# Kernel optimization log

Hardware: AMD Instinct MI355X
Metric: run time of the kernel (lower is better)

## Reference

```python
import jax, jax.numpy as jnp
import numpy as np

N = 50000      # nodes
E = 1600000    # edges (avg degree 32)
C_IN = 128
C_H = 128
C_OUT = 10
G = 512        # number of graphs in the batch


def setup_inputs() -> dict:
    key = jax.random.key(0)
    ks = jax.random.split(key, 16)
    x = jax.random.normal(ks[0], (N, C_IN), dtype=jnp.float32)
    edge_index = jax.random.randint(ks[1], (2, E), 0, N, dtype=jnp.int64)
    batch = jnp.sort(jax.random.randint(ks[2], (N,), 0, G, dtype=jnp.int64))

    def lin(k, fan_in, fan_out):
        lim = 1.0 / np.sqrt(fan_in)
        return jax.random.uniform(k, (fan_in, fan_out), jnp.float32, -lim, lim)

    return {
        "x": x, "edge_index": edge_index, "batch": batch,
        # conv1: c_in -> c_hidden
        "Wr1": lin(ks[3], C_IN, C_H), "br1": jnp.zeros((C_H,), jnp.float32),
        "Wo1": lin(ks[4], C_IN, C_H),
        # conv2: c_hidden -> 2*c_hidden
        "Wr2": lin(ks[5], C_H, 2 * C_H), "br2": jnp.zeros((2 * C_H,), jnp.float32),
        "Wo2": lin(ks[6], C_H, 2 * C_H),
        # conv3: 2*c_hidden -> c_hidden
        "Wr3": lin(ks[7], 2 * C_H, C_H), "br3": jnp.zeros((C_H,), jnp.float32),
        "Wo3": lin(ks[8], 2 * C_H, C_H),
        # head
        "W1": lin(ks[9], C_H, 4 * C_OUT), "b1": jnp.zeros((4 * C_OUT,), jnp.float32),
        "W2": lin(ks[10], 4 * C_OUT, C_OUT), "b2": jnp.zeros((C_OUT,), jnp.float32),
    }


def _graph_conv(x, src, dst, Wr, br, Wo):
    # PyG GraphConv: lin_rel(sum_{j in N(i)} x_j) + lin_root(x_i)
    agg = jax.ops.segment_sum(x[src], dst, num_segments=N)  # [N, F_in]
    return agg @ Wr + br + x @ Wo


def reference(x, edge_index, batch, Wr1, br1, Wo1, Wr2, br2, Wo2,
              Wr3, br3, Wo3, W1, b1, W2, b2):
    src, dst = edge_index[0], edge_index[1]
    h = jax.nn.relu(_graph_conv(x, src, dst, Wr1, br1, Wo1))
    h = jax.nn.relu(_graph_conv(h, src, dst, Wr2, br2, Wo2))
    h = _graph_conv(h, src, dst, Wr3, br3, Wo3)
    # global mean pool over graphs
    sums = jax.ops.segment_sum(h, batch, num_segments=G)            # [G, C_H]
    cnts = jax.ops.segment_sum(jnp.ones((N,), h.dtype), batch, num_segments=G)
    pooled = sums / jnp.maximum(cnts, 1.0)[:, None]
    # dropout is identity in eval mode
    out = pooled @ W1 + b1
    out = out @ W2 + b2
    return out
```

## Files before the change

### kernel.cpp

```cpp
#include <hip/hip_runtime.h>
#include <hip/hip_bf16.h>
#include <cstddef>

#define NN 50000
#define EE 1600000
#define GG 512
#define NB 196
#define BSTRIDE 16384
#define BCAP 10240
#define XBLKS 6250
#define SCBLKS 782
#define PSEG 8

typedef unsigned int u32;
typedef unsigned short u16;
typedef __attribute__((ext_vector_type(8))) short frag_ab;
typedef __attribute__((ext_vector_type(4))) float frag_cd;

__device__ __forceinline__ void gl_lds16(const void* g, void* l) {
    __builtin_amdgcn_global_load_lds(
        (const __attribute__((address_space(1))) u32*)g,
        (__attribute__((address_space(3))) u32*)l, 16, 0, 0);
}
__device__ __forceinline__ float b2f_lo(u32 v) { return __uint_as_float(v << 16); }
__device__ __forceinline__ float b2f_hi(u32 v) { return __uint_as_float(v & 0xffff0000u); }
__device__ __forceinline__ float b2f(u32 v, int odd) { return odd ? b2f_hi(v) : b2f_lo(v); }
__device__ __forceinline__ u16 f2b(float x) {
    __hip_bfloat16 h = __float2bfloat16(x);
    return *(u16*)&h;
}
__device__ __forceinline__ u32 pack2(float lo, float hi) {
    return ((u32)f2b(hi) << 16) | f2b(lo);
}
__device__ __forceinline__ void acc2(float2& a, u32 v) {
    a.x += b2f_lo(v);
    a.y += b2f_hi(v);
}

__device__ inline int lower_bound_i(const int* a, int n, int v) {
    int lo = 0, hi = n;
    while (lo < hi) {
        int m = (lo + hi) >> 1;
        if (a[m] < v) lo = m + 1; else hi = m;
    }
    return lo;
}



__global__ __launch_bounds__(256) void bscatter_prep_kernel(
    const int* __restrict__ ei, int* __restrict__ bcnt, u32* __restrict__ pairs,
    const float* __restrict__ x, u16* __restrict__ ax,
    const float* __restrict__ Wr1, const float* __restrict__ Wo1,
    const float* __restrict__ Wr2, const float* __restrict__ Wo2,
    const float* __restrict__ Wr3, const float* __restrict__ Wo3,
    const float* __restrict__ br3,
    u16* __restrict__ BT1, u16* __restrict__ BT2, u16* __restrict__ BT3,
    float* __restrict__ bias3, const int* __restrict__ batch,
    int* __restrict__ gn) {
    __shared__ int lcnt[NB];
    __shared__ int lbase[NB];
    __shared__ unsigned short lpos[2048];
    int bid = blockIdx.x, t = threadIdx.x;
    if (bid < SCBLKS) {
        int e0 = bid * 2048;
        u32 pk[8];
        int bk[8];
        for (int i = t; i < NB; i += 256) lcnt[i] = 0;
        __syncthreads();
#pragma unroll
        for (int i = 0; i < 8; ++i) {
            int e = e0 + i * 256 + t;
            if (e < EE) {
                int dst = ei[EE + e], src = ei[e];
                int b = dst >> 8;
                bk[i] = b;
                pk[i] = ((u32)src << 8) | (u32)(dst & 255);
                lpos[i * 256 + t] = (unsigned short)atomicAdd(&lcnt[b], 1);
            } else bk[i] = -1;
        }
        __syncthreads();
        for (int i = t; i < NB; i += 256) lbase[i] = atomicAdd(&bcnt[i], lcnt[i]);
        __syncthreads();
#pragma unroll
        for (int i = 0; i < 8; ++i) {
            if (bk[i] >= 0) {
                int pos = lbase[bk[i]] + (int)lpos[i * 256 + t];
                pairs[(size_t)bk[i] * BSTRIDE + pos] = pk[i];
            }
        }
    } else if (bid < SCBLKS + XBLKS) {
        int idx = (bid - SCBLKS) * 256 + t;
        int row = idx >> 5, q = idx & 31;
        float4 v = *(const float4*)(x + (size_t)row * 128 + q * 4);
        *(u32*)(ax + (size_t)row * 256 + 128 + q * 4) = pack2(v.x, v.y);
        *(u32*)(ax + (size_t)row * 256 + 128 + q * 4 + 2) = pack2(v.z, v.w);
    } else if (bid < SCBLKS + XBLKS + 256) {
        int m = bid - SCBLKS - XBLKS;
        int k = t;
        BT2[m * 256 + k] = f2b(k < 128 ? Wr2[k * 256 + m] : Wo2[(k - 128) * 256 + m]);
        BT3[m * 256 + k] = f2b(m < 128 ? Wr3[k * 128 + m] : Wo3[k * 128 + (m - 128)]);
        if (m < 128)
            BT1[m * 256 + k] = f2b(k < 128 ? Wr1[k * 128 + m] : Wo1[(k - 128) * 128 + m]);
        if (k == 0) bias3[m] = (m < 128) ? 0.f : br3[m - 128];
    } else {
        int g = (bid - SCBLKS - XBLKS - 256) * 256 + t;
        if (g <= GG) gn[g] = lower_bound_i(batch, NN, g);
    }
}


__global__ __launch_bounds__(512) void bfill_kernel(const u32* __restrict__ pairs,
                                                    const int* __restrict__ bcnt,
                                                    int* __restrict__ ofs,
                                                    u16* __restrict__ srcl) {
    __shared__ int sc[256];
    __shared__ int cnts[256];
    __shared__ int lcnt[256];
    __shared__ int lcur[256];
    __shared__ int lbuf[BCAP];
    int b = blockIdx.x, t = threadIdx.x;
    if (t < 256) {
        int c = (t < NB) ? bcnt[t] : 0;
        cnts[t] = c;
        sc[t] = c;
        lcnt[t] = 0;
    }
    __syncthreads();
    for (int off = 1; off < 256; off <<= 1) {
        int v = (t >= off && t < 256) ? sc[t - off] : 0;
        __syncthreads();
        if (t < 256) sc[t] += v;
        __syncthreads();
    }
    int base = sc[b] - cnts[b];
    int span = cnts[b];
    const u32* pp = pairs + (size_t)b * BSTRIDE;
    for (int j = t; j < span; j += 512) atomicAdd(&lcnt[pp[j] & 255u], 1);
    __syncthreads();
    int nc = 0;
    if (t < 256) {
        nc = lcnt[t];
        sc[t] = nc;
    }
    __syncthreads();
    for (int off = 1; off < 256; off <<= 1) {
        int v = (t >= off && t < 256) ? sc[t - off] : 0;
        __syncthreads();
        if (t < 256) sc[t] += v;
        __syncthreads();
    }
    if (t < 256) {
        int excl = sc[t] - nc;
        int node = b * 256 + t;
        if (node < NN) ofs[node] = base + excl;
        lcur[t] = excl;
    }
    if (b == 0 && t == 256) ofs[NN] = EE;
    __syncthreads();
    for (int j = t; j < span; j += 512) {
        u32 p = pp[j];
        int pos = atomicAdd(&lcur[p & 255u], 1);
        int src = (int)(p >> 8);
        if (pos < BCAP) lbuf[pos] = src;
        else srcl[base + pos] = (u16)src;
    }
    __syncthreads();
    int lim = span < BCAP ? span : BCAP;
    for (int j = t; j < lim; j += 512) srcl[base + j] = (u16)lbuf[j];
}


__global__ __launch_bounds__(256) void pull_bf_kernel(const u32* __restrict__ Xu,
                                                      const int* __restrict__ ofs,
                                                      const u16* __restrict__ srcl,
                                                      u32* __restrict__ outu) {
    int node = (blockIdx.x * 256 + threadIdx.x) >> 6;
    int lane = threadIdx.x & 63;
    int q = lane >> 4, l = lane & 15;
    int lo = ofs[node], hi = ofs[node + 1];
    float2 a0 = {0.f, 0.f}, a1 = {0.f, 0.f}, a2 = {0.f, 0.f}, a3 = {0.f, 0.f};
    int j = lo;
    for (; j + 15 < hi; j += 16) {
        int s0 = srcl[j + q], s1 = srcl[j + 4 + q];
        int s2 = srcl[j + 8 + q], s3 = srcl[j + 12 + q];
        uint4 v0 = *(const uint4*)(Xu + (size_t)s0 * 128 + l * 4);
        uint4 v1 = *(const uint4*)(Xu + (size_t)s1 * 128 + l * 4);
        uint4 v2 = *(const uint4*)(Xu + (size_t)s2 * 128 + l * 4);
        uint4 v3 = *(const uint4*)(Xu + (size_t)s3 * 128 + l * 4);
        acc2(a0, v0.x); acc2(a1, v0.y); acc2(a2, v0.z); acc2(a3, v0.w);
        acc2(a0, v1.x); acc2(a1, v1.y); acc2(a2, v1.z); acc2(a3, v1.w);
        acc2(a0, v2.x); acc2(a1, v2.y); acc2(a2, v2.z); acc2(a3, v2.w);
        acc2(a0, v3.x); acc2(a1, v3.y); acc2(a2, v3.z); acc2(a3, v3.w);
    }
    for (; j + 3 < hi; j += 4) {
        int s = srcl[j + q];
        uint4 v = *(const uint4*)(Xu + (size_t)s * 128 + l * 4);
        acc2(a0, v.x); acc2(a1, v.y); acc2(a2, v.z); acc2(a3, v.w);
    }
    if (j + q < hi) {
        int s = srcl[j + q];
        uint4 v = *(const uint4*)(Xu + (size_t)s * 128 + l * 4);
        acc2(a0, v.x); acc2(a1, v.y); acc2(a2, v.z); acc2(a3, v.w);
    }
    float acc[8] = {a0.x, a0.y, a1.x, a1.y, a2.x, a2.y, a3.x, a3.y};
#pragma unroll
    for (int i = 0; i < 8; ++i) {
        acc[i] += __shfl_xor(acc[i], 16, 64);
        acc[i] += __shfl_xor(acc[i], 32, 64);
    }
    if (q == 0) {
        uint4 r;
        r.x = pack2(acc[0], acc[1]);
        r.y = pack2(acc[2], acc[3]);
        r.z = pack2(acc[4], acc[5]);
        r.w = pack2(acc[6], acc[7]);
        *(uint4*)(outu + (size_t)node * 128 + l * 4) = r;
    }
}


__global__ __launch_bounds__(256, 2) void gemm_bf_kernel(
    const u16* __restrict__ A, const u16* __restrict__ BT,
    const float* __restrict__ bias, u16* __restrict__ C,
    int ldc, int coloff, int relu) {
    __shared__ alignas(16) u16 As[128 * 32];
    __shared__ alignas(16) u16 Bs[128 * 32];
    const int t = threadIdx.x;
    const int lane = t & 63, wid = t >> 6;
    const int quad = lane >> 4, l16 = lane & 15;
    const int wm = wid >> 1, wn = wid & 1;
    const int row0 = blockIdx.y * 128, c0 = blockIdx.x * 128;

    frag_cd acc[4][4];
#pragma unroll
    for (int i = 0; i < 4; ++i)
#pragma unroll
        for (int j = 0; j < 4; ++j) acc[i][j] = (frag_cd)0.f;

    const int ca = t, cb = t + 256;
    const int ra = ca >> 2, oa = (ca & 3) * 8;
    const int rb = cb >> 2, ob = (cb & 3) * 8;
    const int garow = min(row0 + ra, NN - 1);
    const int gbrow = min(row0 + rb, NN - 1);
    const size_t gA1 = (size_t)garow * 256 + oa;
    const size_t gA2 = (size_t)gbrow * 256 + ob;
    const size_t gB1 = (size_t)(c0 + ra) * 256 + oa;
    const size_t gB2 = (size_t)(c0 + rb) * 256 + ob;

    for (int kk = 0; kk < 256; kk += 32) {
        __syncthreads();
        gl_lds16(A + gA1 + kk, &As[ca * 8]);
        gl_lds16(A + gA2 + kk, &As[cb * 8]);
        gl_lds16(BT + gB1 + kk, &Bs[ca * 8]);
        gl_lds16(BT + gB2 + kk, &Bs[cb * 8]);
        __syncthreads();

        frag_ab a[4], b[4];
#pragma unroll
        for (int mt = 0; mt < 4; ++mt)
            a[mt] = *(const frag_ab*)&As[(wm * 64 + mt * 16 + l16) * 32 + quad * 8];
#pragma unroll
        for (int nt = 0; nt < 4; ++nt)
            b[nt] = *(const frag_ab*)&Bs[(wn * 64 + nt * 16 + l16) * 32 + quad * 8];
#pragma unroll
        for (int mt = 0; mt < 4; ++mt)
#pragma unroll
            for (int nt = 0; nt < 4; ++nt)
                acc[mt][nt] = __builtin_amdgcn_mfma_f32_16x16x32_bf16(
                    a[mt], b[nt], acc[mt][nt], 0, 0, 0);
    }

#pragma unroll
    for (int nt = 0; nt < 4; ++nt) {
        int col = c0 + wn * 64 + nt * 16 + l16;
        float bv = bias[col];
#pragma unroll
        for (int mt = 0; mt < 4; ++mt) {
#pragma unroll
            for (int r = 0; r < 4; ++r) {
                int row = row0 + wm * 64 + mt * 16 + quad * 4 + r;
                if (row < NN) {
                    float v = acc[mt][nt][r] + bv;
                    if (relu) v = fmaxf(v, 0.f);
                    C[(size_t)row * ldc + coloff + col] = f2b(v);
                }
            }
        }
    }
}


__global__ __launch_bounds__(256, 3) void gemm23_kernel(
    const u16* __restrict__ A, const u16* __restrict__ BT2,
    const float* __restrict__ br2, const u16* __restrict__ BT3,
    const float* __restrict__ bias3, u16* __restrict__ C) {
    __shared__ alignas(16) u16 As[64 * 32];
    __shared__ alignas(16) u16 Bs[256 * 32];
    __shared__ alignas(16) u16 Hs[64 * 256];
    const int t = threadIdx.x;
    const int lane = t & 63, w = t >> 6;
    const int quad = lane >> 4, l16 = lane & 15;
    const int row0 = blockIdx.x * 64;

    const int ra = t >> 2, oa = (t & 3) * 8;
    const int garow = min(row0 + ra, NN - 1);
    const size_t gA = (size_t)garow * 256 + oa;
    size_t gB[4];
#pragma unroll
    for (int i = 0; i < 4; ++i) {
        int cbi = i * 256 + t;
        gB[i] = (size_t)(cbi >> 2) * 256 + (cbi & 3) * 8;
    }

    frag_cd acc[16];
#pragma unroll
    for (int i = 0; i < 16; ++i) acc[i] = (frag_cd)0.f;

    for (int kk = 0; kk < 256; kk += 32) {
        __syncthreads();
        gl_lds16(A + gA + kk, &As[t * 8]);
#pragma unroll
        for (int i = 0; i < 4; ++i)
            gl_lds16(BT2 + gB[i] + kk, &Bs[(i * 256 + t) * 8]);
        __syncthreads();
        frag_ab a = *(const frag_ab*)&As[(w * 16 + l16) * 32 + quad * 8];
#pragma unroll
        for (int nt = 0; nt < 16; ++nt) {
            frag_ab b = *(const frag_ab*)&Bs[(nt * 16 + l16) * 32 + quad * 8];
            acc[nt] = __builtin_amdgcn_mfma_f32_16x16x32_bf16(a, b, acc[nt], 0, 0, 0);
        }
    }
#pragma unroll
    for (int nt = 0; nt < 16; ++nt) {
        int col = nt * 16 + l16;
        float bv = br2[col];
#pragma unroll
        for (int r = 0; r < 4; ++r) {
            int lr = w * 16 + quad * 4 + r;
            float v = fmaxf(acc[nt][r] + bv, 0.f);
            Hs[(lr * 256 + col) ^ ((lr & 7) << 3)] = f2b(v);
        }
    }

#pragma unroll
    for (int i = 0; i < 16; ++i) acc[i] = (frag_cd)0.f;
    const int hrow = w * 16 + l16;
    for (int kk = 0; kk < 256; kk += 32) {
        __syncthreads();
#pragma unroll
        for (int i = 0; i < 4; ++i)
            gl_lds16(BT3 + gB[i] + kk, &Bs[(i * 256 + t) * 8]);
        __syncthreads();
        frag_ab a = *(const frag_ab*)&Hs[(hrow * 256 + kk + quad * 8) ^
                                         ((hrow & 7) << 3)];
#pragma unroll
        for (int nt = 0; nt < 16; ++nt) {
            frag_ab b = *(const frag_ab*)&Bs[(nt * 16 + l16) * 32 + quad * 8];
            acc[nt] = __builtin_amdgcn_mfma_f32_16x16x32_bf16(a, b, acc[nt], 0, 0, 0);
        }
    }

#pragma unroll
    for (int nt = 0; nt < 16; ++nt) {
        int col = nt * 16 + l16;
        float bv = bias3[col];
#pragma unroll
        for (int r = 0; r < 4; ++r) {
            int lr = w * 16 + quad * 4 + r;
            Hs[(lr * 256 + col) ^ ((lr & 7) << 3)] = f2b(acc[nt][r] + bv);
        }
    }
    __syncthreads();
    const uint4* Hs128 = (const uint4*)Hs;
#pragma unroll
    for (int it = 0; it < 8; ++it) {
        int row = it * 8 + (t >> 5);
        int grp = t & 31;
        uint4 v = Hs128[row * 32 + (grp ^ (row & 7))];
        int grow = row0 + row;
        if (grow < NN)
            *(uint4*)(C + (size_t)grow * 256 + grp * 8) = v;
    }
}


__global__ __launch_bounds__(256) void pool3_seg_kernel(
    const u32* __restrict__ Tu, const int* __restrict__ ofs,
    const u16* __restrict__ srcl, const int* __restrict__ gn,
    float* __restrict__ psum) {
    __shared__ float red[4][128];
    __shared__ float po[2][128];
    int gb = blockIdx.x;
    int g = gb >> 3, s = gb & 7;
    int t = threadIdx.x;
    int w = t >> 6, lane = t & 63;
    int q = lane >> 4, l = lane & 15;
    int n_lo = gn[g], n_hi = gn[g + 1];
    int glo = ofs[n_lo], ghi = ofs[n_hi];
    int len = ghi - glo;
    int s_lo = glo + (int)(((long long)len * s) >> 3);
    int s_hi = glo + (int)(((long long)len * (s + 1)) >> 3);
    int slen = s_hi - s_lo;
    int wlo = s_lo + ((slen * w) >> 2);
    int whi = s_lo + ((slen * (w + 1)) >> 2);

    float2 a0 = {0.f, 0.f}, a1 = {0.f, 0.f}, a2 = {0.f, 0.f}, a3 = {0.f, 0.f};
    int j = wlo;
    for (; j + 15 < whi; j += 16) {
        int s0 = srcl[j + q], s1 = srcl[j + 4 + q];
        int s2 = srcl[j + 8 + q], s3 = srcl[j + 12 + q];
        uint4 v0 = *(const uint4*)(Tu + (size_t)s0 * 128 + l * 4);
        uint4 v1 = *(const uint4*)(Tu + (size_t)s1 * 128 + l * 4);
        uint4 v2 = *(const uint4*)(Tu + (size_t)s2 * 128 + l * 4);
        uint4 v3 = *(const uint4*)(Tu + (size_t)s3 * 128 + l * 4);
        acc2(a0, v0.x); acc2(a1, v0.y); acc2(a2, v0.z); acc2(a3, v0.w);
        acc2(a0, v1.x); acc2(a1, v1.y); acc2(a2, v1.z); acc2(a3, v1.w);
        acc2(a0, v2.x); acc2(a1, v2.y); acc2(a2, v2.z); acc2(a3, v2.w);
        acc2(a0, v3.x); acc2(a1, v3.y); acc2(a2, v3.z); acc2(a3, v3.w);
    }
    for (; j + 3 < whi; j += 4) {
        int sv = srcl[j + q];
        uint4 v = *(const uint4*)(Tu + (size_t)sv * 128 + l * 4);
        acc2(a0, v.x); acc2(a1, v.y); acc2(a2, v.z); acc2(a3, v.w);
    }
    if (j + q < whi) {
        int sv = srcl[j + q];
        uint4 v = *(const uint4*)(Tu + (size_t)sv * 128 + l * 4);
        acc2(a0, v.x); acc2(a1, v.y); acc2(a2, v.z); acc2(a3, v.w);
    }
    float acc[8] = {a0.x, a0.y, a1.x, a1.y, a2.x, a2.y, a3.x, a3.y};
#pragma unroll
    for (int i = 0; i < 8; ++i) {
        acc[i] += __shfl_xor(acc[i], 16, 64);
        acc[i] += __shfl_xor(acc[i], 32, 64);
    }
    if (q == 0) {
#pragma unroll
        for (int i = 0; i < 8; ++i) red[w][l * 8 + i] = acc[i];
    }
    float so = 0.f;
    int ch = t & 127, rg = t >> 7;
    for (int r = n_lo + s * 2 + rg; r < n_hi; r += 16)
        so += b2f(Tu[(size_t)r * 128 + 64 + (ch >> 1)], ch & 1);
    po[rg][ch] = so;
    __syncthreads();
    if (t < 128) {
        float v = red[0][t] + red[1][t] + red[2][t] + red[3][t] + po[0][t] + po[1][t];
        psum[((size_t)g * PSEG + s) * 128 + t] = v;
    }
}


__global__ __launch_bounds__(128) void head_kernel(
    const float* __restrict__ psum, const int* __restrict__ gn,
    const float* __restrict__ W1, const float* __restrict__ b1,
    const float* __restrict__ W2, const float* __restrict__ b2,
    float* __restrict__ out) {
    __shared__ float p[128];
    __shared__ float hid[40];
    int g = blockIdx.x, t = threadIdx.x;
    int cnt = gn[g + 1] - gn[g];
    float sv = 0.f;
#pragma unroll
    for (int k = 0; k < PSEG; ++k) sv += psum[((size_t)g * PSEG + k) * 128 + t];
    p[t] = sv / fmaxf((float)cnt, 1.f);
    __syncthreads();
    if (t < 40) {
        float v = b1[t];
        for (int k = 0; k < 128; ++k) v += p[k] * W1[k * 40 + t];
        hid[t] = v;
    }
    __syncthreads();
    if (t < 10) {
        float v = b2[t];
        for (int j = 0; j < 40; ++j) v += hid[j] * W2[j * 10 + t];
        out[g * 10 + t] = v;
    }
}


extern "C" void kernel_launch(void* const* d_in, const int* in_sizes, int n_in,
                              void* d_out, int out_size, void* d_ws, size_t ws_size,
                              hipStream_t stream) {
    const float* x   = (const float*)d_in[0];
    const int* ei    = (const int*)d_in[1];
    const int* batch = (const int*)d_in[2];
    const float* Wr1 = (const float*)d_in[3];
    const float* br1 = (const float*)d_in[4];
    const float* Wo1 = (const float*)d_in[5];
    const float* Wr2 = (const float*)d_in[6];
    const float* br2 = (const float*)d_in[7];
    const float* Wo2 = (const float*)d_in[8];
    const float* Wr3 = (const float*)d_in[9];
    const float* br3 = (const float*)d_in[10];
    const float* Wo3 = (const float*)d_in[11];
    const float* W1  = (const float*)d_in[12];
    const float* b1  = (const float*)d_in[13];
    const float* W2  = (const float*)d_in[14];
    const float* b2  = (const float*)d_in[15];
    float* out = (float*)d_out;

    char* ws = (char*)d_ws;
    size_t off = 0;
    auto alloc = [&](size_t bytes) {
        void* p = ws + off;
        off += (bytes + 255) & ~(size_t)255;
        return p;
    };
    int* ofs      = (int*)alloc((NN + 1) * sizeof(int));
    int* bcnt     = (int*)alloc(256 * sizeof(int));
    int* gn       = (int*)alloc((GG + 1) * sizeof(int));
    u16* srcl     = (u16*)alloc((size_t)EE * 2);
    u16* ax       = (u16*)alloc((size_t)NN * 256 * 2);
    u16* ah1      = (u16*)alloc((size_t)NN * 256 * 2);
    u16* t3o3     = (u16*)alloc((size_t)NN * 256 * 2);
    float* psum   = (float*)alloc((size_t)GG * PSEG * 128 * sizeof(float));
    u16* BT1      = (u16*)alloc(128 * 256 * 2);
    u16* BT2      = (u16*)alloc(256 * 256 * 2);
    u16* BT3      = (u16*)alloc(256 * 256 * 2);
    float* bias3  = (float*)alloc(256 * sizeof(float));
    u32* pairs = (u32*)t3o3;

    hipMemsetAsync(bcnt, 0, 256 * sizeof(int), stream);

    bscatter_prep_kernel<<<SCBLKS + XBLKS + 256 + 3, 256, 0, stream>>>(
        ei, bcnt, pairs, x, ax, Wr1, Wo1, Wr2, Wo2, Wr3, Wo3, br3,
        BT1, BT2, BT3, bias3, batch, gn);
    bfill_kernel<<<NB, 512, 0, stream>>>(pairs, bcnt, ofs, srcl);

    pull_bf_kernel<<<NN * 64 / 256, 256, 0, stream>>>((const u32*)ax + 64, ofs, srcl, (u32*)ax);
    gemm_bf_kernel<<<dim3(1, 391), 256, 0, stream>>>(ax, BT1, br1, ah1, 256, 128, 1);
    pull_bf_kernel<<<NN * 64 / 256, 256, 0, stream>>>((const u32*)ah1 + 64, ofs, srcl, (u32*)ah1);
    gemm23_kernel<<<782, 256, 0, stream>>>(ah1, BT2, br2, BT3, bias3, t3o3);

    pool3_seg_kernel<<<GG * PSEG, 256, 0, stream>>>((const u32*)t3o3, ofs, srcl, gn, psum);
    head_kernel<<<GG, 128, 0, stream>>>(psum, gn, W1, b1, W2, b2, out);
}
```

Measured before the change: 340.0 us.

## Gather neighbor features from FP8 shadow copies instead of bf16 rows

Each producer (input conversion, layer-1 GEMM, layer-2/3 GEMM) now also writes an FP8 copy of the features that later get gathered along edges. The pull and pool kernels gather these 128-byte FP8 rows instead of 256-byte bf16 rows, which halves the random-gather traffic that dominates the aggregation. The layer-1 GEMM is rewritten as a 64-row tile kernel with an LDS-staged epilogue so it can emit both formats. The cost is extra writes and a large precision loss (FP8 e4m3) on aggregated features, which may break the accuracy tolerance.

```diff
diff --git a/kernel.cpp b/kernel.cpp
--- a/kernel.cpp
+++ b/kernel.cpp
@@ -16,6 +16,7 @@
 typedef unsigned short u16;
 typedef __attribute__((ext_vector_type(8))) short frag_ab;
 typedef __attribute__((ext_vector_type(4))) float frag_cd;
+typedef __attribute__((ext_vector_type(2))) float f32x2;
 
 __device__ __forceinline__ void gl_lds16(const void* g, void* l) {
     __builtin_amdgcn_global_load_lds(
@@ -32,9 +33,14 @@
 __device__ __forceinline__ u32 pack2(float lo, float hi) {
     return ((u32)f2b(hi) << 16) | f2b(lo);
 }
-__device__ __forceinline__ void acc2(float2& a, u32 v) {
-    a.x += b2f_lo(v);
-    a.y += b2f_hi(v);
+__device__ __forceinline__ void accf8(float* a, u32 w) {
+    f32x2 p0 = __builtin_amdgcn_cvt_pk_f32_fp8(w, false);
+    f32x2 p1 = __builtin_amdgcn_cvt_pk_f32_fp8(w, true);
+    a[0] += p0.x; a[1] += p0.y; a[2] += p1.x; a[3] += p1.y;
+}
+__device__ __forceinline__ u32 pk4_f8(float a, float b, float c, float d) {
+    u32 w = __builtin_amdgcn_cvt_pk_fp8_f32(a, b, 0, false);
+    return __builtin_amdgcn_cvt_pk_fp8_f32(c, d, w, true);
 }
 
 __device__ inline int lower_bound_i(const int* a, int n, int v) {
@@ -50,7 +56,7 @@
 
 __global__ __launch_bounds__(256) void bscatter_prep_kernel(
     const int* __restrict__ ei, int* __restrict__ bcnt, u32* __restrict__ pairs,
-    const float* __restrict__ x, u16* __restrict__ ax,
+    const float* __restrict__ x, u16* __restrict__ ax, u32* __restrict__ x8,
     const float* __restrict__ Wr1, const float* __restrict__ Wo1,
     const float* __restrict__ Wr2, const float* __restrict__ Wo2,
     const float* __restrict__ Wr3, const float* __restrict__ Wo3,
@@ -95,6 +101,7 @@
         float4 v = *(const float4*)(x + (size_t)row * 128 + q * 4);
         *(u32*)(ax + (size_t)row * 256 + 128 + q * 4) = pack2(v.x, v.y);
         *(u32*)(ax + (size_t)row * 256 + 128 + q * 4 + 2) = pack2(v.z, v.w);
+        x8[(size_t)row * 32 + q] = pk4_f8(v.x, v.y, v.z, v.w);
     } else if (bid < SCBLKS + XBLKS + 256) {
         int m = bid - SCBLKS - XBLKS;
         int k = t;
@@ -171,121 +178,131 @@
 }
 
 
-__global__ __launch_bounds__(256) void pull_bf_kernel(const u32* __restrict__ Xu,
+__global__ __launch_bounds__(256) void pull_f8_kernel(const u32* __restrict__ X8,
                                                       const int* __restrict__ ofs,
                                                       const u16* __restrict__ srcl,
                                                       u32* __restrict__ outu) {
     int node = (blockIdx.x * 256 + threadIdx.x) >> 6;
     int lane = threadIdx.x & 63;
-    int q = lane >> 4, l = lane & 15;
+    int q = lane >> 3, l = lane & 7;
     int lo = ofs[node], hi = ofs[node + 1];
-    float2 a0 = {0.f, 0.f}, a1 = {0.f, 0.f}, a2 = {0.f, 0.f}, a3 = {0.f, 0.f};
+    float acc[16];
+#pragma unroll
+    for (int i = 0; i < 16; ++i) acc[i] = 0.f;
     int j = lo;
+    for (; j + 31 < hi; j += 32) {
+        int s0 = srcl[j + q], s1 = srcl[j + 8 + q];
+        int s2 = srcl[j + 16 + q], s3 = srcl[j + 24 + q];
+        uint4 v0 = *(const uint4*)(X8 + (size_t)s0 * 32 + l * 4);
+        uint4 v1 = *(const uint4*)(X8 + (size_t)s1 * 32 + l * 4);
+        uint4 v2 = *(const uint4*)(X8 + (size_t)s2 * 32 + l * 4);
+        uint4 v3 = *(const uint4*)(X8 + (size_t)s3 * 32 + l * 4);
+        accf8(acc + 0, v0.x); accf8(acc + 4, v0.y); accf8(acc + 8, v0.z); accf8(acc + 12, v0.w);
+        accf8(acc + 0, v1.x); accf8(acc + 4, v1.y); accf8(acc + 8, v1.z); accf8(acc + 12, v1.w);
+        accf8(acc + 0, v2.x); accf8(acc + 4, v2.y); accf8(acc + 8, v2.z); accf8(acc + 12, v2.w);
+        accf8(acc + 0, v3.x); accf8(acc + 4, v3.y); accf8(acc + 8, v3.z); accf8(acc + 12, v3.w);
+    }
     for (; j + 15 < hi; j += 16) {
-        int s0 = srcl[j + q], s1 = srcl[j + 4 + q];
-        int s2 = srcl[j + 8 + q], s3 = srcl[j + 12 + q];
-        uint4 v0 = *(const uint4*)(Xu + (size_t)s0 * 128 + l * 4);
-        uint4 v1 = *(const uint4*)(Xu + (size_t)s1 * 128 + l * 4);
-        uint4 v2 = *(const uint4*)(Xu + (size_t)s2 * 128 + l * 4);
-        uint4 v3 = *(const uint4*)(Xu + (size_t)s3 * 128 + l * 4);
-        acc2(a0, v0.x); acc2(a1, v0.y); acc2(a2, v0.z); acc2(a3, v0.w);
-        acc2(a0, v1.x); acc2(a1, v1.y); acc2(a2, v1.z); acc2(a3, v1.w);
-        acc2(a0, v2.x); acc2(a1, v2.y); acc2(a2, v2.z); acc2(a3, v2.w);
-        acc2(a0, v3.x); acc2(a1, v3.y); acc2(a2, v3.z); acc2(a3, v3.w);
-    }
-    for (; j + 3 < hi; j += 4) {
+        int s0 = srcl[j + q], s1 = srcl[j + 8 + q];
+        uint4 v0 = *(const uint4*)(X8 + (size_t)s0 * 32 + l * 4);
+        uint4 v1 = *(const uint4*)(X8 + (size_t)s1 * 32 + l * 4);
+        accf8(acc + 0, v0.x); accf8(acc + 4, v0.y); accf8(acc + 8, v0.z); accf8(acc + 12, v0.w);
+        accf8(acc + 0, v1.x); accf8(acc + 4, v1.y); accf8(acc + 8, v1.z); accf8(acc + 12, v1.w);
+    }
+    for (; j + 7 < hi; j += 8) {
         int s = srcl[j + q];
-        uint4 v = *(const uint4*)(Xu + (size_t)s * 128 + l * 4);
-        acc2(a0, v.x); acc2(a1, v.y); acc2(a2, v.z); acc2(a3, v.w);
+        uint4 v = *(const uint4*)(X8 + (size_t)s * 32 + l * 4);
+        accf8(acc + 0, v.x); accf8(acc + 4, v.y); accf8(acc + 8, v.z); accf8(acc + 12, v.w);
     }
     if (j + q < hi) {
         int s = srcl[j + q];
-        uint4 v = *(const uint4*)(Xu + (size_t)s * 128 + l * 4);
-        acc2(a0, v.x); acc2(a1, v.y); acc2(a2, v.z); acc2(a3, v.w);
-    }
-    float acc[8] = {a0.x, a0.y, a1.x, a1.y, a2.x, a2.y, a3.x, a3.y};
-#pragma unroll
-    for (int i = 0; i < 8; ++i) {
+        uint4 v = *(const uint4*)(X8 + (size_t)s * 32 + l * 4);
+        accf8(acc + 0, v.x); accf8(acc + 4, v.y); accf8(acc + 8, v.z); accf8(acc + 12, v.w);
+    }
+#pragma unroll
+    for (int i = 0; i < 16; ++i) {
+        acc[i] += __shfl_xor(acc[i], 8, 64);
         acc[i] += __shfl_xor(acc[i], 16, 64);
         acc[i] += __shfl_xor(acc[i], 32, 64);
     }
     if (q == 0) {
-        uint4 r;
-        r.x = pack2(acc[0], acc[1]);
-        r.y = pack2(acc[2], acc[3]);
-        r.z = pack2(acc[4], acc[5]);
-        r.w = pack2(acc[6], acc[7]);
-        *(uint4*)(outu + (size_t)node * 128 + l * 4) = r;
-    }
-}
-
-
-__global__ __launch_bounds__(256, 2) void gemm_bf_kernel(
-    const u16* __restrict__ A, const u16* __restrict__ BT,
-    const float* __restrict__ bias, u16* __restrict__ C,
-    int ldc, int coloff, int relu) {
-    __shared__ alignas(16) u16 As[128 * 32];
+        uint4 r0, r1;
+        r0.x = pack2(acc[0], acc[1]);  r0.y = pack2(acc[2], acc[3]);
+        r0.z = pack2(acc[4], acc[5]);  r0.w = pack2(acc[6], acc[7]);
+        r1.x = pack2(acc[8], acc[9]);  r1.y = pack2(acc[10], acc[11]);
+        r1.z = pack2(acc[12], acc[13]); r1.w = pack2(acc[14], acc[15]);
+        *(uint4*)(outu + (size_t)node * 128 + l * 8) = r0;
+        *(uint4*)(outu + (size_t)node * 128 + l * 8 + 4) = r1;
+    }
+}
+
+
+__global__ __launch_bounds__(256, 3) void gemm1_kernel(
+    const u16* __restrict__ A, const u16* __restrict__ BT1,
+    const float* __restrict__ br1, u16* __restrict__ C, u32* __restrict__ F8) {
+    __shared__ alignas(16) u16 As[64 * 32];
     __shared__ alignas(16) u16 Bs[128 * 32];
+    __shared__ alignas(16) u16 Hs[64 * 128];
     const int t = threadIdx.x;
-    const int lane = t & 63, wid = t >> 6;
+    const int lane = t & 63, w = t >> 6;
     const int quad = lane >> 4, l16 = lane & 15;
-    const int wm = wid >> 1, wn = wid & 1;
-    const int row0 = blockIdx.y * 128, c0 = blockIdx.x * 128;
-
-    frag_cd acc[4][4];
-#pragma unroll
-    for (int i = 0; i < 4; ++i)
-#pragma unroll
-        for (int j = 0; j < 4; ++j) acc[i][j] = (frag_cd)0.f;
-
-    const int ca = t, cb = t + 256;
-    const int ra = ca >> 2, oa = (ca & 3) * 8;
-    const int rb = cb >> 2, ob = (cb & 3) * 8;
+    const int row0 = blockIdx.x * 64;
+
+    const int ra = t >> 2, oa = (t & 3) * 8;
     const int garow = min(row0 + ra, NN - 1);
-    const int gbrow = min(row0 + rb, NN - 1);
-    const size_t gA1 = (size_t)garow * 256 + oa;
-    const size_t gA2 = (size_t)gbrow * 256 + ob;
-    const size_t gB1 = (size_t)(c0 + ra) * 256 + oa;
-    const size_t gB2 = (size_t)(c0 + rb) * 256 + ob;
+    const size_t gA = (size_t)garow * 256 + oa;
+    size_t gB[2];
+#pragma unroll
+    for (int i = 0; i < 2; ++i) {
+        int cbi = i * 256 + t;
+        gB[i] = (size_t)(cbi >> 2) * 256 + (cbi & 3) * 8;
+    }
+
+    frag_cd acc[8];
+#pragma unroll
+    for (int i = 0; i < 8; ++i) acc[i] = (frag_cd)0.f;
 
     for (int kk = 0; kk < 256; kk += 32) {
         __syncthreads();
-        gl_lds16(A + gA1 + kk, &As[ca * 8]);
-        gl_lds16(A + gA2 + kk, &As[cb * 8]);
-        gl_lds16(BT + gB1 + kk, &Bs[ca * 8]);
-        gl_lds16(BT + gB2 + kk, &Bs[cb * 8]);
-        __syncthreads();
-
-        frag_ab a[4], b[4];
-#pragma unroll
-        for (int mt = 0; mt < 4; ++mt)
-            a[mt] = *(const frag_ab*)&As[(wm * 64 + mt * 16 + l16) * 32 + quad * 8];
-#pragma unroll
-        for (int nt = 0; nt < 4; ++nt)
-            b[nt] = *(const frag_ab*)&Bs[(wn * 64 + nt * 16 + l16) * 32 + quad * 8];
-#pragma unroll
-        for (int mt = 0; mt < 4; ++mt)
-#pragma unroll
-            for (int nt = 0; nt < 4; ++nt)
-                acc[mt][nt] = __builtin_amdgcn_mfma_f32_16x16x32_bf16(
-                    a[mt], b[nt], acc[mt][nt], 0, 0, 0);
-    }
-
-#pragma unroll
-    for (int nt = 0; nt < 4; ++nt) {
-        int col = c0 + wn * 64 + nt * 16 + l16;
-        float bv = bias[col];
-#pragma unroll
-        for (int mt = 0; mt < 4; ++mt) {
-#pragma unroll
-            for (int r = 0; r < 4; ++r) {
-                int row = row0 + wm * 64 + mt * 16 + quad * 4 + r;
-                if (row < NN) {
-                    float v = acc[mt][nt][r] + bv;
-                    if (relu) v = fmaxf(v, 0.f);
-                    C[(size_t)row * ldc + coloff + col] = f2b(v);
-                }
-            }
+        gl_lds16(A + gA + kk, &As[t * 8]);
+#pragma unroll
+        for (int i = 0; i < 2; ++i)
+            gl_lds16(BT1 + gB[i] + kk, &Bs[(i * 256 + t) * 8]);
+        __syncthreads();
+        frag_ab a = *(const frag_ab*)&As[(w * 16 + l16) * 32 + quad * 8];
+#pragma unroll
+        for (int nt = 0; nt < 8; ++nt) {
+            frag_ab b = *(const frag_ab*)&Bs[(nt * 16 + l16) * 32 + quad * 8];
+            acc[nt] = __builtin_amdgcn_mfma_f32_16x16x32_bf16(a, b, acc[nt], 0, 0, 0);
+        }
+    }
+#pragma unroll
+    for (int nt = 0; nt < 8; ++nt) {
+        int col = nt * 16 + l16;
+        float bv = br1[col];
+#pragma unroll
+        for (int r = 0; r < 4; ++r) {
+            int lr = w * 16 + quad * 4 + r;
+            float v = fmaxf(acc[nt][r] + bv, 0.f);
+            Hs[(lr * 128 + col) ^ ((lr & 7) << 3)] = f2b(v);
+        }
+    }
+    __syncthreads();
+    const uint4* Hs128 = (const uint4*)Hs;
+#pragma unroll
+    for (int it = 0; it < 4; ++it) {
+        int row = it * 16 + (t >> 4);
+        int grp = t & 15;
+        uint4 v = Hs128[row * 16 + (grp ^ (row & 7))];
+        int grow = row0 + row;
+        if (grow < NN) {
+            *(uint4*)(C + (size_t)grow * 256 + 128 + grp * 8) = v;
+            float f0 = b2f_lo(v.x), f1 = b2f_hi(v.x), f2 = b2f_lo(v.y), f3 = b2f_hi(v.y);
+            float f4 = b2f_lo(v.z), f5 = b2f_hi(v.z), f6 = b2f_lo(v.w), f7 = b2f_hi(v.w);
+            uint2 w8;
+            w8.x = pk4_f8(f0, f1, f2, f3);
+            w8.y = pk4_f8(f4, f5, f6, f7);
+            *(uint2*)(F8 + (size_t)grow * 32 + grp * 2) = w8;
         }
     }
 }
@@ -294,7 +311,7 @@
 __global__ __launch_bounds__(256, 3) void gemm23_kernel(
     const u16* __restrict__ A, const u16* __restrict__ BT2,
     const float* __restrict__ br2, const u16* __restrict__ BT3,
-    const float* __restrict__ bias3, u16* __restrict__ C) {
+    const float* __restrict__ bias3, u16* __restrict__ C, u32* __restrict__ T8) {
     __shared__ alignas(16) u16 As[64 * 32];
     __shared__ alignas(16) u16 Bs[256 * 32];
     __shared__ alignas(16) u16 Hs[64 * 256];
@@ -379,23 +396,32 @@
         int grp = t & 31;
         uint4 v = Hs128[row * 32 + (grp ^ (row & 7))];
         int grow = row0 + row;
-        if (grow < NN)
+        if (grow < NN) {
             *(uint4*)(C + (size_t)grow * 256 + grp * 8) = v;
-    }
-}
-
-
-__global__ __launch_bounds__(256) void pool3_seg_kernel(
-    const u32* __restrict__ Tu, const int* __restrict__ ofs,
-    const u16* __restrict__ srcl, const int* __restrict__ gn,
-    float* __restrict__ psum) {
+            if (grp < 16) {
+                float f0 = b2f_lo(v.x), f1 = b2f_hi(v.x), f2 = b2f_lo(v.y), f3 = b2f_hi(v.y);
+                float f4 = b2f_lo(v.z), f5 = b2f_hi(v.z), f6 = b2f_lo(v.w), f7 = b2f_hi(v.w);
+                uint2 w8;
+                w8.x = pk4_f8(f0, f1, f2, f3);
+                w8.y = pk4_f8(f4, f5, f6, f7);
+                *(uint2*)(T8 + (size_t)grow * 32 + grp * 2) = w8;
+            }
+        }
+    }
+}
+
+
+__global__ __launch_bounds__(256) void pool3_f8_kernel(
+    const u32* __restrict__ T8, const u32* __restrict__ Tu,
+    const int* __restrict__ ofs, const u16* __restrict__ srcl,
+    const int* __restrict__ gn, float* __restrict__ psum) {
     __shared__ float red[4][128];
     __shared__ float po[2][128];
     int gb = blockIdx.x;
     int g = gb >> 3, s = gb & 7;
     int t = threadIdx.x;
     int w = t >> 6, lane = t & 63;
-    int q = lane >> 4, l = lane & 15;
+    int q = lane >> 3, l = lane & 7;
     int n_lo = gn[g], n_hi = gn[g + 1];
     int glo = ofs[n_lo], ghi = ofs[n_hi];
     int len = ghi - glo;
@@ -405,39 +431,48 @@
     int wlo = s_lo + ((slen * w) >> 2);
     int whi = s_lo + ((slen * (w + 1)) >> 2);
 
-    float2 a0 = {0.f, 0.f}, a1 = {0.f, 0.f}, a2 = {0.f, 0.f}, a3 = {0.f, 0.f};
+    float acc[16];
+#pragma unroll
+    for (int i = 0; i < 16; ++i) acc[i] = 0.f;
     int j = wlo;
+    for (; j + 31 < whi; j += 32) {
+        int s0 = srcl[j + q], s1 = srcl[j + 8 + q];
+        int s2 = srcl[j + 16 + q], s3 = srcl[j + 24 + q];
+        uint4 v0 = *(const uint4*)(T8 + (size_t)s0 * 32 + l * 4);
+        uint4 v1 = *(const uint4*)(T8 + (size_t)s1 * 32 + l * 4);
+        uint4 v2 = *(const uint4*)(T8 + (size_t)s2 * 32 + l * 4);
+        uint4 v3 = *(const uint4*)(T8 + (size_t)s3 * 32 + l * 4);
+        accf8(acc + 0, v0.x); accf8(acc + 4, v0.y); accf8(acc + 8, v0.z); accf8(acc + 12, v0.w);
+        accf8(acc + 0, v1.x); accf8(acc + 4, v1.y); accf8(acc + 8, v1.z); accf8(acc + 12, v1.w);
+        accf8(acc + 0, v2.x); accf8(acc + 4, v2.y); accf8(acc + 8, v2.z); accf8(acc + 12, v2.w);
+        accf8(acc + 0, v3.x); accf8(acc + 4, v3.y); accf8(acc + 8, v3.z); accf8(acc + 12, v3.w);
+    }
     for (; j + 15 < whi; j += 16) {
-        int s0 = srcl[j + q], s1 = srcl[j + 4 + q];
-        int s2 = srcl[j + 8 + q], s3 = srcl[j + 12 + q];
-        uint4 v0 = *(const uint4*)(Tu + (size_t)s0 * 128 + l * 4);
-        uint4 v1 = *(const uint4*)(Tu + (size_t)s1 * 128 + l * 4);
-        uint4 v2 = *(const uint4*)(Tu + (size_t)s2 * 128 + l * 4);
-        uint4 v3 = *(const uint4*)(Tu + (size_t)s3 * 128 + l * 4);
-        acc2(a0, v0.x); acc2(a1, v0.y); acc2(a2, v0.z); acc2(a3, v0.w);
-        acc2(a0, v1.x); acc2(a1, v1.y); acc2(a2, v1.z); acc2(a3, v1.w);
-        acc2(a0, v2.x); acc2(a1, v2.y); acc2(a2, v2.z); acc2(a3, v2.w);
-        acc2(a0, v3.x); acc2(a1, v3.y); acc2(a2, v3.z); acc2(a3, v3.w);
-    }
-    for (; j + 3 < whi; j += 4) {
+        int s0 = srcl[j + q], s1 = srcl[j + 8 + q];
+        uint4 v0 = *(const uint4*)(T8 + (size_t)s0 * 32 + l * 4);
+        uint4 v1 = *(const uint4*)(T8 + (size_t)s1 * 32 + l * 4);
+        accf8(acc + 0, v0.x); accf8(acc + 4, v0.y); accf8(acc + 8, v0.z); accf8(acc + 12, v0.w);
+        accf8(acc + 0, v1.x); accf8(acc + 4, v1.y); accf8(acc + 8, v1.z); accf8(acc + 12, v1.w);
+    }
+    for (; j + 7 < whi; j += 8) {
         int sv = srcl[j + q];
-        uint4 v = *(const uint4*)(Tu + (size_t)sv * 128 + l * 4);
-        acc2(a0, v.x); acc2(a1, v.y); acc2(a2, v.z); acc2(a3, v.w);
+        uint4 v = *(const uint4*)(T8 + (size_t)sv * 32 + l * 4);
+        accf8(acc + 0, v.x); accf8(acc + 4, v.y); accf8(acc + 8, v.z); accf8(acc + 12, v.w);
     }
     if (j + q < whi) {
         int sv = srcl[j + q];
-        uint4 v = *(const uint4*)(Tu + (size_t)sv * 128 + l * 4);
-        acc2(a0, v.x); acc2(a1, v.y); acc2(a2, v.z); acc2(a3, v.w);
-    }
-    float acc[8] = {a0.x, a0.y, a1.x, a1.y, a2.x, a2.y, a3.x, a3.y};
-#pragma unroll
-    for (int i = 0; i < 8; ++i) {
+        uint4 v = *(const uint4*)(T8 + (size_t)sv * 32 + l * 4);
+        accf8(acc + 0, v.x); accf8(acc + 4, v.y); accf8(acc + 8, v.z); accf8(acc + 12, v.w);
+    }
+#pragma unroll
+    for (int i = 0; i < 16; ++i) {
+        acc[i] += __shfl_xor(acc[i], 8, 64);
         acc[i] += __shfl_xor(acc[i], 16, 64);
         acc[i] += __shfl_xor(acc[i], 32, 64);
     }
     if (q == 0) {
 #pragma unroll
-        for (int i = 0; i < 8; ++i) red[w][l * 8 + i] = acc[i];
+        for (int i = 0; i < 16; ++i) red[w][l * 16 + i] = acc[i];
     }
     float so = 0.f;
     int ch = t & 127, rg = t >> 7;
@@ -515,6 +550,9 @@
     u16* ax       = (u16*)alloc((size_t)NN * 256 * 2);
     u16* ah1      = (u16*)alloc((size_t)NN * 256 * 2);
     u16* t3o3     = (u16*)alloc((size_t)NN * 256 * 2);
+    u32* x8       = (u32*)alloc((size_t)NN * 128);
+    u32* h1f8     = (u32*)alloc((size_t)NN * 128);
+    u32* t3f8     = (u32*)alloc((size_t)NN * 128);
     float* psum   = (float*)alloc((size_t)GG * PSEG * 128 * sizeof(float));
     u16* BT1      = (u16*)alloc(128 * 256 * 2);
     u16* BT2      = (u16*)alloc(256 * 256 * 2);
@@ -525,15 +563,16 @@
     hipMemsetAsync(bcnt, 0, 256 * sizeof(int), stream);
 
     bscatter_prep_kernel<<<SCBLKS + XBLKS + 256 + 3, 256, 0, stream>>>(
-        ei, bcnt, pairs, x, ax, Wr1, Wo1, Wr2, Wo2, Wr3, Wo3, br3,
+        ei, bcnt, pairs, x, ax, x8, Wr1, Wo1, Wr2, Wo2, Wr3, Wo3, br3,
         BT1, BT2, BT3, bias3, batch, gn);
     bfill_kernel<<<NB, 512, 0, stream>>>(pairs, bcnt, ofs, srcl);
 
-    pull_bf_kernel<<<NN * 64 / 256, 256, 0, stream>>>((const u32*)ax + 64, ofs, srcl, (u32*)ax);
-    gemm_bf_kernel<<<dim3(1, 391), 256, 0, stream>>>(ax, BT1, br1, ah1, 256, 128, 1);
-    pull_bf_kernel<<<NN * 64 / 256, 256, 0, stream>>>((const u32*)ah1 + 64, ofs, srcl, (u32*)ah1);
-    gemm23_kernel<<<782, 256, 0, stream>>>(ah1, BT2, br2, BT3, bias3, t3o3);
-
-    pool3_seg_kernel<<<GG * PSEG, 256, 0, stream>>>((const u32*)t3o3, ofs, srcl, gn, psum);
+    pull_f8_kernel<<<NN * 64 / 256, 256, 0, stream>>>(x8, ofs, srcl, (u32*)ax);
+    gemm1_kernel<<<782, 256, 0, stream>>>(ax, BT1, br1, ah1, h1f8);
+    pull_f8_kernel<<<NN * 64 / 256, 256, 0, stream>>>(h1f8, ofs, srcl, (u32*)ah1);
+    gemm23_kernel<<<782, 256, 0, stream>>>(ah1, BT2, br2, BT3, bias3, t3o3, t3f8);
+
+    pool3_f8_kernel<<<GG * PSEG, 256, 0, stream>>>(t3f8, (const u32*)t3o3,
+                                                   ofs, srcl, gn, psum);
     head_kernel<<<GG, 128, 0, stream>>>(psum, gn, W1, b1, W2, b2, out);
 }
```

After: 301.1 us. -11.4%, faster.
